# Kernel tuning notes

Hardware: AMD Instinct MI355X
Metric: run time of the kernel (lower is better)

## Reference

```python
import jax, jax.numpy as jnp
import numpy as np

DIM = 96
NUM_HEADS = 3
WIN = 7  # window_size (square)


def _relative_position_index(wh, ww):
    coords = np.stack(np.meshgrid(np.arange(wh), np.arange(ww), indexing='ij'))  # [2, wh, ww]
    flat = coords.reshape(2, -1)  # [2, n]
    rel = flat[:, :, None] - flat[:, None, :]  # [2, n, n]
    rel = rel.transpose(1, 2, 0).astype(np.int64)
    rel[..., 0] += wh - 1
    rel[..., 1] += ww - 1
    rel[..., 0] *= 2 * ww - 1
    return rel.sum(-1)  # [n, n]


def setup_inputs() -> dict:
    key = jax.random.key(0)
    ks = jax.random.split(key, 9)
    b, n, c = 8192, WIN * WIN, DIM
    std = 0.02
    inp = {
        'x': jax.random.normal(ks[0], (b, n, c), jnp.float32),
        'v': jax.random.normal(ks[1], (b, n, c), jnp.float32),
        'w_q': jax.random.normal(ks[2], (c, c), jnp.float32) * std,
        'b_q': jnp.zeros((c,), jnp.float32),
        'w_kv': jax.random.normal(ks[3], (c, 2 * c), jnp.float32) * std,
        'b_kv': jnp.zeros((2 * c,), jnp.float32),
        'w_proj': jax.random.normal(ks[4], (c, c), jnp.float32) * std,
        'b_proj': jnp.zeros((c,), jnp.float32),
        'rpb_table': jax.random.normal(ks[5], ((2 * WIN - 1) * (2 * WIN - 1), NUM_HEADS), jnp.float32) * std,
        'rel_index': jnp.asarray(_relative_position_index(WIN, WIN), jnp.int32),
    }
    return inp


def reference(x, v, w_q, b_q, w_kv, b_kv, w_proj, b_proj, rpb_table, rel_index):
    b, n, c = x.shape
    h = NUM_HEADS
    hd = c // h
    scale = hd ** -0.5
    # q: [b, h, n, hd]
    q = (x @ w_q + b_q).reshape(b, n, h, hd).transpose(0, 2, 1, 3) * scale
    kv = (v @ w_kv + b_kv).reshape(b, n, 2, h, hd)
    k = kv[:, :, 0].transpose(0, 2, 1, 3)  # [b, h, n, hd]
    vv = kv[:, :, 1].transpose(0, 2, 1, 3)
    attn = jnp.einsum('bhqd,bhkd->bhqk', q, k)  # [b, h, n, n]
    bias = rpb_table[rel_index.reshape(-1)].reshape(n, n, h).transpose(2, 0, 1)  # [h, n, n]
    attn = jax.nn.softmax(attn + bias[None], axis=-1)
    out = jnp.einsum('bhqk,bhkd->bhqd', attn, vv).transpose(0, 2, 1, 3).reshape(b, n, c)
    return out @ w_proj + b_proj
```

## Files before the change

### kernel.cpp

```cpp
#include <hip/hip_runtime.h>
#include <hip/hip_bf16.h>

typedef __bf16 bf16x8 __attribute__((ext_vector_type(8)));
typedef float f32x4 __attribute__((ext_vector_type(4)));
typedef short s16x8 __attribute__((ext_vector_type(8)));
typedef short s16x4 __attribute__((ext_vector_type(4)));

#define NTOK 49
#define CDIM 96
#define KS_S 104
#define VT_S 56
#define BN_S 136
#define LOG2E 1.4426950408889634f

#if __has_builtin(__builtin_amdgcn_exp2f)
#define EXP2F(x) __builtin_amdgcn_exp2f(x)
#else
#define EXP2F(x) exp2f(x)
#endif

#define DRAIN() do { asm volatile("s_waitcnt lgkmcnt(0)" ::: "memory"); \
                     __builtin_amdgcn_sched_barrier(0); } while (0)

__device__ __forceinline__ unsigned short f2bf(float f) {
  __hip_bfloat16 h = __float2bfloat16(f);
  return __builtin_bit_cast(unsigned short, h);
}

__device__ __forceinline__ bf16x8 ld_cvt8(const float* p) {
  float4 a = *(const float4*)p;
  float4 b = *(const float4*)(p + 4);
  s16x8 r;
  r[0] = (short)f2bf(a.x); r[1] = (short)f2bf(a.y);
  r[2] = (short)f2bf(a.z); r[3] = (short)f2bf(a.w);
  r[4] = (short)f2bf(b.x); r[5] = (short)f2bf(b.y);
  r[6] = (short)f2bf(b.z); r[7] = (short)f2bf(b.w);
  return __builtin_bit_cast(bf16x8, r);
}

__global__ void prep(const float* __restrict__ wq, const float* __restrict__ wkv,
                     const float* __restrict__ wproj, const float* __restrict__ rpb,
                     const int* __restrict__ relidx, unsigned short* __restrict__ wsT,
                     float* __restrict__ biasf) {
  const int total = 36864 + 3 * 49 * 64;
  for (int i = blockIdx.x * 256 + threadIdx.x; i < total; i += gridDim.x * 256) {
    if (i < 9216) {
      int oc = i / 96, ic = i - oc * 96;
      wsT[i] = f2bf(wq[ic * 96 + oc]);
    } else if (i < 27648) {
      int j = i - 9216; int oc = j / 96, ic = j - oc * 96;
      wsT[i] = f2bf(wkv[ic * 192 + oc]);
    } else if (i < 36864) {
      int j = i - 27648; int oc = j / 96, ic = j - oc * 96;
      wsT[i] = f2bf(wproj[ic * 96 + oc]);
    } else {
      int j = i - 36864; int h = j / 3136; int rc = j - h * 3136;
      int r = rc >> 6, c = rc & 63;
      biasf[j] = (c < 49) ? rpb[relidx[r * 49 + c] * 3 + h] * LOG2E : 0.f;
    }
  }
}

__launch_bounds__(256, 4)
__global__ void attn_fused(const float* __restrict__ xg, const float* __restrict__ vg,
                           const float* __restrict__ bq, const float* __restrict__ bkv,
                           const float* __restrict__ bproj,
                           const unsigned short* __restrict__ wsT,
                           const float* __restrict__ biasf,
                           float* __restrict__ outg) {
  __shared__ __align__(16) unsigned char smem[38352];
  unsigned short* Ks  = (unsigned short*)smem;
  unsigned short* VVT = (unsigned short*)(smem + 10192);

  const int tid = threadIdx.x;
  const int lane = tid & 63;
  const int wv = tid >> 6;
  const int c16 = lane & 15;
  const int g4 = lane >> 4;
  const int win = blockIdx.x;
  const int q0 = (wv == 0) ? 0 : (wv == 1) ? 16 : (wv == 2) ? 32 : 33;
  unsigned short* bnc = (unsigned short*)(smem + 20944) + wv * (16 * BN_S);

  const int mp = wv & 1;
  const bool isK = (wv < 2);
  const int m0 = mp ? 32 : 0;
  const int m1 = mp ? 33 : 16;

  const float* base = xg + (size_t)win * (NTOK * CDIM);
  const float* vbase = vg + (size_t)win * (NTOK * CDIM);
  const float* xrow = base + (q0 + c16) * CDIM;
  const float* vrow0 = vbase + (m0 + c16) * CDIM;
  const float* vrow1 = vbase + (m1 + c16) * CDIM;

  bf16x8 xf[3], vf0[3], vf1[3];
#pragma unroll
  for (int k = 0; k < 3; ++k) {
    xf[k]  = ld_cvt8(xrow  + k * 32 + g4 * 8);
    vf0[k] = ld_cvt8(vrow0 + k * 32 + g4 * 8);
    vf1[k] = ld_cvt8(vrow1 + k * 32 + g4 * 8);
  }

  const float scale = 0.2550348742f;
#pragma unroll
  for (int nt = 0; nt < 6; ++nt) {
    f32x4 acc = {0, 0, 0, 0};
    const int ocl = nt * 16 + c16;
#pragma unroll
    for (int k = 0; k < 3; ++k) {
      bf16x8 b = *(const bf16x8*)(wsT + ocl * 96 + k * 32 + g4 * 8);
      acc = __builtin_amdgcn_mfma_f32_16x16x32_bf16(xf[k], b, acc, 0, 0, 0);
    }
    float bias = bq[ocl];
#pragma unroll
    for (int r = 0; r < 4; ++r)
      bnc[(4 * g4 + r) * BN_S + ocl] = f2bf((acc[r] + bias) * scale);
  }

#pragma unroll
  for (int nt = 0; nt < 6; ++nt) {
    const int ocl = (isK ? 0 : 96) + nt * 16 + c16;
    f32x4 a0 = {0, 0, 0, 0}, a1 = {0, 0, 0, 0};
#pragma unroll
    for (int k = 0; k < 3; ++k) {
      bf16x8 b = *(const bf16x8*)(wsT + 9216 + ocl * 96 + k * 32 + g4 * 8);
      a0 = __builtin_amdgcn_mfma_f32_16x16x32_bf16(vf0[k], b, a0, 0, 0, 0);
      a1 = __builtin_amdgcn_mfma_f32_16x16x32_bf16(vf1[k], b, a1, 0, 0, 0);
    }
    float bias = bkv[ocl];
    if (isK) {
#pragma unroll
      for (int r = 0; r < 4; ++r)
        Ks[(m0 + 4 * g4 + r) * KS_S + ocl] = f2bf(a0[r] + bias);
#pragma unroll
      for (int r = 0; r < 4; ++r)
        Ks[(m1 + 4 * g4 + r) * KS_S + ocl] = f2bf(a1[r] + bias);
    } else {
      int dim = ocl - 96;
      s16x4 p0;
#pragma unroll
      for (int r = 0; r < 4; ++r) p0[r] = (short)f2bf(a0[r] + bias);
      *(s16x4*)(VVT + dim * VT_S + (m0 + 4 * g4)) = p0;
      if (mp == 0) {
        s16x4 p1;
#pragma unroll
        for (int r = 0; r < 4; ++r) p1[r] = (short)f2bf(a1[r] + bias);
        *(s16x4*)(VVT + dim * VT_S + (16 + 4 * g4)) = p1;
      } else {
#pragma unroll
        for (int r = 0; r < 4; ++r)
          VVT[dim * VT_S + 33 + 4 * g4 + r] = f2bf(a1[r] + bias);
      }
    }
  }
  __syncthreads();

  const int q = q0 + c16;

  s16x8 vmask;
#pragma unroll
  for (int j = 0; j < 8; ++j)
    vmask[j] = (short)(((32 + g4 * 8 + j) < 49) ? 0xFFFF : 0x0000);

  f32x4 oacc[6] = {{0,0,0,0},{0,0,0,0},{0,0,0,0},{0,0,0,0},{0,0,0,0},{0,0,0,0}};

  auto softmax_pw = [&](const f32x4* s, const f32x4* bv, int pcol) {
    float vals[16];
#pragma unroll
    for (int kt = 0; kt < 4; ++kt)
#pragma unroll
      for (int r = 0; r < 4; ++r) {
        int key = 16 * kt + 4 * g4 + r;
        vals[kt * 4 + r] = (kt < 3 || key < 49) ? (s[kt][r] + bv[kt][r]) : -1e30f;
      }
    float m8[8];
#pragma unroll
    for (int j = 0; j < 8; ++j) m8[j] = fmaxf(vals[j], vals[j + 8]);
    float ma = fmaxf(m8[0], m8[4]), mb = fmaxf(m8[1], m8[5]);
    float mc = fmaxf(m8[2], m8[6]), md = fmaxf(m8[3], m8[7]);
    float mx = fmaxf(fmaxf(ma, mb), fmaxf(mc, md));
    mx = fmaxf(mx, __shfl_xor(mx, 16, 64));
    mx = fmaxf(mx, __shfl_xor(mx, 32, 64));
    float e[16];
#pragma unroll
    for (int j = 0; j < 16; ++j) e[j] = EXP2F(vals[j] - mx);
    float s8[8];
#pragma unroll
    for (int j = 0; j < 8; ++j) s8[j] = e[j] + e[j + 8];
    float sa = s8[0] + s8[4], sb = s8[1] + s8[5], sc = s8[2] + s8[6], sd = s8[3] + s8[7];
    float sum = (sa + sb) + (sc + sd);
    sum += __shfl_xor(sum, 16, 64);
    sum += __shfl_xor(sum, 32, 64);
    float rinv = 1.0f / sum;
#pragma unroll
    for (int kt = 0; kt < 4; ++kt) {
      s16x4 p;
#pragma unroll
      for (int r = 0; r < 4; ++r) p[r] = (short)f2bf(e[kt * 4 + r] * rinv);
      *(s16x4*)(bnc + c16 * BN_S + pcol + 16 * kt + 4 * g4) = p;
    }
  };

  auto pv_out = [&](int h, int pcol, int ocol) {
    bf16x8 ap0 = *(const bf16x8*)(bnc + c16 * BN_S + pcol + g4 * 8);
    bf16x8 ap1 = *(const bf16x8*)(bnc + c16 * BN_S + pcol + 32 + g4 * 8);
#pragma unroll
    for (int dt = 0; dt < 2; ++dt) {
      int dim = h * 32 + dt * 16 + c16;
      bf16x8 bv0 = *(const bf16x8*)(VVT + dim * VT_S + g4 * 8);
      s16x8 b1 = *(const s16x8*)(VVT + dim * VT_S + 32 + g4 * 8);
      b1 &= vmask;
      f32x4 o = __builtin_amdgcn_mfma_f32_16x16x32_bf16(ap0, bv0, (f32x4){0,0,0,0}, 0, 0, 0);
      o = __builtin_amdgcn_mfma_f32_16x16x32_bf16(ap1, __builtin_bit_cast(bf16x8, b1), o, 0, 0, 0);
#pragma unroll
      for (int r = 0; r < 4; ++r)
        bnc[(4 * g4 + r) * BN_S + ocol + dt * 16 + c16] = f2bf(o[r]);
    }
  };

  auto oproj = [&](int h, int ocol) {
    bf16x8 bo = *(const bf16x8*)(bnc + c16 * BN_S + ocol + g4 * 8);
#pragma unroll
    for (int mt = 0; mt < 6; ++mt) {
      bf16x8 a = *(const bf16x8*)(wsT + 27648 + (mt * 16 + c16) * 96 + h * 32 + g4 * 8);
      oacc[mt] = __builtin_amdgcn_mfma_f32_16x16x32_bf16(a, bo, oacc[mt], 0, 0, 0);
    }
  };

  f32x4 b0v[4], b1v[4];
  {
    const float* br0 = biasf + q * 64 + 4 * g4;
    const float* br1 = biasf + (49 + q) * 64 + 4 * g4;
#pragma unroll
    for (int kt = 0; kt < 4; ++kt) {
      b0v[kt] = *(const f32x4*)(br0 + 16 * kt);
      b1v[kt] = *(const f32x4*)(br1 + 16 * kt);
    }
  }
  bf16x8 qf0 = *(const bf16x8*)(bnc + c16 * BN_S + g4 * 8);
  bf16x8 qf1 = *(const bf16x8*)(bnc + c16 * BN_S + 32 + g4 * 8);
  bf16x8 qf2 = *(const bf16x8*)(bnc + c16 * BN_S + 64 + g4 * 8);

  f32x4 s0[4], s1[4];
#pragma unroll
  for (int kt = 0; kt < 4; ++kt) {
    bf16x8 ak = *(const bf16x8*)(Ks + (16 * kt + c16) * KS_S + g4 * 8);
    s0[kt] = __builtin_amdgcn_mfma_f32_16x16x32_bf16(ak, qf0, (f32x4){0,0,0,0}, 0, 0, 0);
  }
#pragma unroll
  for (int kt = 0; kt < 4; ++kt) {
    bf16x8 ak = *(const bf16x8*)(Ks + (16 * kt + c16) * KS_S + 32 + g4 * 8);
    s1[kt] = __builtin_amdgcn_mfma_f32_16x16x32_bf16(ak, qf1, (f32x4){0,0,0,0}, 0, 0, 0);
  }
  softmax_pw(s0, b0v, 0);
  softmax_pw(s1, b1v, 64);

  f32x4 b2v[4];
  {
    const float* br2 = biasf + (98 + q) * 64 + 4 * g4;
#pragma unroll
    for (int kt = 0; kt < 4; ++kt) b2v[kt] = *(const f32x4*)(br2 + 16 * kt);
  }
  f32x4 s2[4];
#pragma unroll
  for (int kt = 0; kt < 4; ++kt) {
    bf16x8 ak = *(const bf16x8*)(Ks + (16 * kt + c16) * KS_S + 64 + g4 * 8);
    s2[kt] = __builtin_amdgcn_mfma_f32_16x16x32_bf16(ak, qf2, (f32x4){0,0,0,0}, 0, 0, 0);
  }

  DRAIN();
  pv_out(0, 0, 0);
  pv_out(1, 64, 32);
  softmax_pw(s2, b2v, 64);

  DRAIN();
  oproj(0, 0);
  oproj(1, 32);
  pv_out(2, 64, 96);

  DRAIN();
  oproj(2, 96);

  {
    const bool store_ok = (wv < 3) || (c16 == 15);
    float* orow = outg + (size_t)win * (NTOK * CDIM) + q * 96;
#pragma unroll
    for (int mt = 0; mt < 6; ++mt) {
      int oc0 = mt * 16 + g4 * 4;
      if (store_ok) {
        float4 bb = *(const float4*)(bproj + oc0);
        float4 o4;
        o4.x = oacc[mt][0] + bb.x; o4.y = oacc[mt][1] + bb.y;
        o4.z = oacc[mt][2] + bb.z; o4.w = oacc[mt][3] + bb.w;
        *(float4*)(orow + oc0) = o4;
      }
    }
  }
}

extern "C" void kernel_launch(void* const* d_in, const int* in_sizes, int n_in,
                              void* d_out, int out_size, void* d_ws, size_t ws_size,
                              hipStream_t stream) {
  const float* x     = (const float*)d_in[0];
  const float* v     = (const float*)d_in[1];
  const float* wq    = (const float*)d_in[2];
  const float* bq    = (const float*)d_in[3];
  const float* wkv   = (const float*)d_in[4];
  const float* bkv   = (const float*)d_in[5];
  const float* wproj = (const float*)d_in[6];
  const float* bproj = (const float*)d_in[7];
  const float* rpb   = (const float*)d_in[8];
  const int*   relidx= (const int*)d_in[9];
  float* out = (float*)d_out;
  unsigned short* wsT = (unsigned short*)d_ws;
  float* biasf = (float*)((char*)d_ws + 73728);
  int nwin = in_sizes[0] / (NTOK * CDIM);

  hipLaunchKernelGGL(prep, dim3(181), dim3(256), 0, stream,
                     wq, wkv, wproj, rpb, relidx, wsT, biasf);
  hipLaunchKernelGGL(attn_fused, dim3(nwin), dim3(256), 0, stream,
                     x, v, bq, bkv, bproj, wsT, biasf, out);
}
```

Measured before the change: 251.0 us.

## Fuse Q/KV projection loops with weight prefetch, packed bf16 converts, and setprio

```diff
diff --git a/kernel.cpp b/kernel.cpp
--- a/kernel.cpp
+++ b/kernel.cpp
@@ -27,15 +27,27 @@
   return __builtin_bit_cast(unsigned short, h);
 }
 
+__device__ __forceinline__ unsigned int cvtpk(float lo, float hi) {
+  unsigned int r;
+  asm("v_cvt_pk_bf16_f32 %0, %1, %2" : "=v"(r) : "v"(lo), "v"(hi));
+  return r;
+}
+__device__ __forceinline__ unsigned short f2bf_f(float f) {
+  return (unsigned short)cvtpk(f, f);
+}
+__device__ __forceinline__ s16x4 pack4(float a, float b, float c, float d) {
+  union { unsigned int u[2]; s16x4 v; } r;
+  r.u[0] = cvtpk(a, b); r.u[1] = cvtpk(c, d);
+  return r.v;
+}
+
 __device__ __forceinline__ bf16x8 ld_cvt8(const float* p) {
   float4 a = *(const float4*)p;
   float4 b = *(const float4*)(p + 4);
-  s16x8 r;
-  r[0] = (short)f2bf(a.x); r[1] = (short)f2bf(a.y);
-  r[2] = (short)f2bf(a.z); r[3] = (short)f2bf(a.w);
-  r[4] = (short)f2bf(b.x); r[5] = (short)f2bf(b.y);
-  r[6] = (short)f2bf(b.z); r[7] = (short)f2bf(b.w);
-  return __builtin_bit_cast(bf16x8, r);
+  union { unsigned int u[4]; bf16x8 v; } r;
+  r.u[0] = cvtpk(a.x, a.y); r.u[1] = cvtpk(a.z, a.w);
+  r.u[2] = cvtpk(b.x, b.y); r.u[3] = cvtpk(b.z, b.w);
+  return r.v;
 }
 
 __global__ void prep(const float* __restrict__ wq, const float* __restrict__ wkv,
@@ -61,7 +73,7 @@
   }
 }
 
-__launch_bounds__(256, 4)
+__launch_bounds__(256, 3)
 __global__ void attn_fused(const float* __restrict__ xg, const float* __restrict__ vg,
                            const float* __restrict__ bq, const float* __restrict__ bkv,
                            const float* __restrict__ bproj,
@@ -72,11 +84,8 @@
   unsigned short* Ks  = (unsigned short*)smem;
   unsigned short* VVT = (unsigned short*)(smem + 10192);
 
-  const int tid = threadIdx.x;
-  const int lane = tid & 63;
-  const int wv = tid >> 6;
-  const int c16 = lane & 15;
-  const int g4 = lane >> 4;
+  const int tid = threadIdx.x, lane = tid & 63, wv = tid >> 6;
+  const int c16 = lane & 15, g4 = lane >> 4;
   const int win = blockIdx.x;
   const int q0 = (wv == 0) ? 0 : (wv == 1) ? 16 : (wv == 2) ? 32 : 33;
   unsigned short* bnc = (unsigned short*)(smem + 20944) + wv * (16 * BN_S);
@@ -100,62 +109,78 @@
     vf1[k] = ld_cvt8(vrow1 + k * 32 + g4 * 8);
   }
 
+  float bqv[6], bkvv[6];
+#pragma unroll
+  for (int nt = 0; nt < 6; ++nt) {
+    bqv[nt]  = bq[nt * 16 + c16];
+    bkvv[nt] = bkv[(isK ? 0 : 96) + nt * 16 + c16];
+  }
+
   const float scale = 0.2550348742f;
-#pragma unroll
-  for (int nt = 0; nt < 6; ++nt) {
-    f32x4 acc = {0, 0, 0, 0};
-    const int ocl = nt * 16 + c16;
+  const unsigned short* wkvBase = wsT + 9216 + (isK ? 0 : 9216);
+
+  {
+    bf16x8 wqf[2][3], wkf[2][3];
 #pragma unroll
     for (int k = 0; k < 3; ++k) {
-      bf16x8 b = *(const bf16x8*)(wsT + ocl * 96 + k * 32 + g4 * 8);
-      acc = __builtin_amdgcn_mfma_f32_16x16x32_bf16(xf[k], b, acc, 0, 0, 0);
-    }
-    float bias = bq[ocl];
-#pragma unroll
-    for (int r = 0; r < 4; ++r)
-      bnc[(4 * g4 + r) * BN_S + ocl] = f2bf((acc[r] + bias) * scale);
-  }
-
-#pragma unroll
-  for (int nt = 0; nt < 6; ++nt) {
-    const int ocl = (isK ? 0 : 96) + nt * 16 + c16;
-    f32x4 a0 = {0, 0, 0, 0}, a1 = {0, 0, 0, 0};
-#pragma unroll
-    for (int k = 0; k < 3; ++k) {
-      bf16x8 b = *(const bf16x8*)(wsT + 9216 + ocl * 96 + k * 32 + g4 * 8);
-      a0 = __builtin_amdgcn_mfma_f32_16x16x32_bf16(vf0[k], b, a0, 0, 0, 0);
-      a1 = __builtin_amdgcn_mfma_f32_16x16x32_bf16(vf1[k], b, a1, 0, 0, 0);
-    }
-    float bias = bkv[ocl];
-    if (isK) {
-#pragma unroll
-      for (int r = 0; r < 4; ++r)
-        Ks[(m0 + 4 * g4 + r) * KS_S + ocl] = f2bf(a0[r] + bias);
-#pragma unroll
-      for (int r = 0; r < 4; ++r)
-        Ks[(m1 + 4 * g4 + r) * KS_S + ocl] = f2bf(a1[r] + bias);
-    } else {
-      int dim = ocl - 96;
-      s16x4 p0;
-#pragma unroll
-      for (int r = 0; r < 4; ++r) p0[r] = (short)f2bf(a0[r] + bias);
-      *(s16x4*)(VVT + dim * VT_S + (m0 + 4 * g4)) = p0;
-      if (mp == 0) {
-        s16x4 p1;
-#pragma unroll
-        for (int r = 0; r < 4; ++r) p1[r] = (short)f2bf(a1[r] + bias);
-        *(s16x4*)(VVT + dim * VT_S + (16 + 4 * g4)) = p1;
-      } else {
+      wqf[0][k] = *(const bf16x8*)(wsT     + c16 * 96 + k * 32 + g4 * 8);
+      wkf[0][k] = *(const bf16x8*)(wkvBase + c16 * 96 + k * 32 + g4 * 8);
+    }
+#pragma unroll
+    for (int nt = 0; nt < 6; ++nt) {
+      const int cur = nt & 1, nxt = cur ^ 1;
+      if (nt < 5) {
+#pragma unroll
+        for (int k = 0; k < 3; ++k) {
+          wqf[nxt][k] = *(const bf16x8*)(wsT     + ((nt + 1) * 16 + c16) * 96 + k * 32 + g4 * 8);
+          wkf[nxt][k] = *(const bf16x8*)(wkvBase + ((nt + 1) * 16 + c16) * 96 + k * 32 + g4 * 8);
+        }
+      }
+      f32x4 aq = {0,0,0,0}, a0 = {0,0,0,0}, a1 = {0,0,0,0};
+      __builtin_amdgcn_s_setprio(1);
+#pragma unroll
+      for (int k = 0; k < 3; ++k) {
+        aq = __builtin_amdgcn_mfma_f32_16x16x32_bf16(xf[k],  wqf[cur][k], aq, 0, 0, 0);
+        a0 = __builtin_amdgcn_mfma_f32_16x16x32_bf16(vf0[k], wkf[cur][k], a0, 0, 0, 0);
+        a1 = __builtin_amdgcn_mfma_f32_16x16x32_bf16(vf1[k], wkf[cur][k], a1, 0, 0, 0);
+      }
+      __builtin_amdgcn_s_setprio(0);
+      {
+        const int ocl = nt * 16 + c16;
+        float bias = bqv[nt];
 #pragma unroll
         for (int r = 0; r < 4; ++r)
-          VVT[dim * VT_S + 33 + 4 * g4 + r] = f2bf(a1[r] + bias);
+          bnc[(4 * g4 + r) * BN_S + ocl] = f2bf_f((aq[r] + bias) * scale);
+      }
+      {
+        float bias = bkvv[nt];
+        if (isK) {
+          const int ocl = nt * 16 + c16;
+#pragma unroll
+          for (int r = 0; r < 4; ++r)
+            Ks[(m0 + 4 * g4 + r) * KS_S + ocl] = f2bf_f(a0[r] + bias);
+#pragma unroll
+          for (int r = 0; r < 4; ++r)
+            Ks[(m1 + 4 * g4 + r) * KS_S + ocl] = f2bf_f(a1[r] + bias);
+        } else {
+          const int dim = nt * 16 + c16;
+          *(s16x4*)(VVT + dim * VT_S + (m0 + 4 * g4)) =
+              pack4(a0[0] + bias, a0[1] + bias, a0[2] + bias, a0[3] + bias);
+          if (mp == 0) {
+            *(s16x4*)(VVT + dim * VT_S + (16 + 4 * g4)) =
+                pack4(a1[0] + bias, a1[1] + bias, a1[2] + bias, a1[3] + bias);
+          } else {
+#pragma unroll
+            for (int r = 0; r < 4; ++r)
+              VVT[dim * VT_S + 33 + 4 * g4 + r] = f2bf_f(a1[r] + bias);
+          }
+        }
       }
     }
   }
   __syncthreads();
 
   const int q = q0 + c16;
-
   s16x8 vmask;
 #pragma unroll
   for (int j = 0; j < 8; ++j)
@@ -192,38 +217,48 @@
     sum += __shfl_xor(sum, 32, 64);
     float rinv = 1.0f / sum;
 #pragma unroll
-    for (int kt = 0; kt < 4; ++kt) {
-      s16x4 p;
-#pragma unroll
-      for (int r = 0; r < 4; ++r) p[r] = (short)f2bf(e[kt * 4 + r] * rinv);
-      *(s16x4*)(bnc + c16 * BN_S + pcol + 16 * kt + 4 * g4) = p;
-    }
+    for (int kt = 0; kt < 4; ++kt)
+      *(s16x4*)(bnc + c16 * BN_S + pcol + 16 * kt + 4 * g4) =
+          pack4(e[kt*4] * rinv, e[kt*4+1] * rinv, e[kt*4+2] * rinv, e[kt*4+3] * rinv);
   };
 
   auto pv_out = [&](int h, int pcol, int ocol) {
     bf16x8 ap0 = *(const bf16x8*)(bnc + c16 * BN_S + pcol + g4 * 8);
     bf16x8 ap1 = *(const bf16x8*)(bnc + c16 * BN_S + pcol + 32 + g4 * 8);
+    bf16x8 bva[2]; s16x8 bvb[2];
 #pragma unroll
     for (int dt = 0; dt < 2; ++dt) {
       int dim = h * 32 + dt * 16 + c16;
-      bf16x8 bv0 = *(const bf16x8*)(VVT + dim * VT_S + g4 * 8);
-      s16x8 b1 = *(const s16x8*)(VVT + dim * VT_S + 32 + g4 * 8);
-      b1 &= vmask;
-      f32x4 o = __builtin_amdgcn_mfma_f32_16x16x32_bf16(ap0, bv0, (f32x4){0,0,0,0}, 0, 0, 0);
-      o = __builtin_amdgcn_mfma_f32_16x16x32_bf16(ap1, __builtin_bit_cast(bf16x8, b1), o, 0, 0, 0);
+      bva[dt] = *(const bf16x8*)(VVT + dim * VT_S + g4 * 8);
+      s16x8 t = *(const s16x8*)(VVT + dim * VT_S + 32 + g4 * 8);
+      bvb[dt] = t & vmask;
+    }
+    f32x4 o[2];
+    __builtin_amdgcn_s_setprio(1);
+#pragma unroll
+    for (int dt = 0; dt < 2; ++dt) {
+      o[dt] = __builtin_amdgcn_mfma_f32_16x16x32_bf16(ap0, bva[dt], (f32x4){0,0,0,0}, 0, 0, 0);
+      o[dt] = __builtin_amdgcn_mfma_f32_16x16x32_bf16(ap1, __builtin_bit_cast(bf16x8, bvb[dt]), o[dt], 0, 0, 0);
+    }
+    __builtin_amdgcn_s_setprio(0);
+#pragma unroll
+    for (int dt = 0; dt < 2; ++dt)
 #pragma unroll
       for (int r = 0; r < 4; ++r)
-        bnc[(4 * g4 + r) * BN_S + ocol + dt * 16 + c16] = f2bf(o[r]);
-    }
+        bnc[(4 * g4 + r) * BN_S + ocol + dt * 16 + c16] = f2bf_f(o[dt][r]);
   };
 
   auto oproj = [&](int h, int ocol) {
     bf16x8 bo = *(const bf16x8*)(bnc + c16 * BN_S + ocol + g4 * 8);
-#pragma unroll
-    for (int mt = 0; mt < 6; ++mt) {
-      bf16x8 a = *(const bf16x8*)(wsT + 27648 + (mt * 16 + c16) * 96 + h * 32 + g4 * 8);
-      oacc[mt] = __builtin_amdgcn_mfma_f32_16x16x32_bf16(a, bo, oacc[mt], 0, 0, 0);
-    }
+    bf16x8 wa[6];
+#pragma unroll
+    for (int mt = 0; mt < 6; ++mt)
+      wa[mt] = *(const bf16x8*)(wsT + 27648 + (mt * 16 + c16) * 96 + h * 32 + g4 * 8);
+    __builtin_amdgcn_s_setprio(1);
+#pragma unroll
+    for (int mt = 0; mt < 6; ++mt)
+      oacc[mt] = __builtin_amdgcn_mfma_f32_16x16x32_bf16(wa[mt], bo, oacc[mt], 0, 0, 0);
+    __builtin_amdgcn_s_setprio(0);
   };
 
   f32x4 b0v[4], b1v[4];
@@ -241,15 +276,21 @@
   bf16x8 qf2 = *(const bf16x8*)(bnc + c16 * BN_S + 64 + g4 * 8);
 
   f32x4 s0[4], s1[4];
-#pragma unroll
-  for (int kt = 0; kt < 4; ++kt) {
-    bf16x8 ak = *(const bf16x8*)(Ks + (16 * kt + c16) * KS_S + g4 * 8);
-    s0[kt] = __builtin_amdgcn_mfma_f32_16x16x32_bf16(ak, qf0, (f32x4){0,0,0,0}, 0, 0, 0);
-  }
-#pragma unroll
-  for (int kt = 0; kt < 4; ++kt) {
-    bf16x8 ak = *(const bf16x8*)(Ks + (16 * kt + c16) * KS_S + 32 + g4 * 8);
-    s1[kt] = __builtin_amdgcn_mfma_f32_16x16x32_bf16(ak, qf1, (f32x4){0,0,0,0}, 0, 0, 0);
+  {
+    bf16x8 ak0[4], ak1[4];
+#pragma unroll
+    for (int kt = 0; kt < 4; ++kt) {
+      ak0[kt] = *(const bf16x8*)(Ks + (16 * kt + c16) * KS_S + g4 * 8);
+      ak1[kt] = *(const bf16x8*)(Ks + (16 * kt + c16) * KS_S + 32 + g4 * 8);
+    }
+    __builtin_amdgcn_s_setprio(1);
+#pragma unroll
+    for (int kt = 0; kt < 4; ++kt)
+      s0[kt] = __builtin_amdgcn_mfma_f32_16x16x32_bf16(ak0[kt], qf0, (f32x4){0,0,0,0}, 0, 0, 0);
+#pragma unroll
+    for (int kt = 0; kt < 4; ++kt)
+      s1[kt] = __builtin_amdgcn_mfma_f32_16x16x32_bf16(ak1[kt], qf1, (f32x4){0,0,0,0}, 0, 0, 0);
+    __builtin_amdgcn_s_setprio(0);
   }
   softmax_pw(s0, b0v, 0);
   softmax_pw(s1, b1v, 64);
@@ -261,10 +302,16 @@
     for (int kt = 0; kt < 4; ++kt) b2v[kt] = *(const f32x4*)(br2 + 16 * kt);
   }
   f32x4 s2[4];
-#pragma unroll
-  for (int kt = 0; kt < 4; ++kt) {
-    bf16x8 ak = *(const bf16x8*)(Ks + (16 * kt + c16) * KS_S + 64 + g4 * 8);
-    s2[kt] = __builtin_amdgcn_mfma_f32_16x16x32_bf16(ak, qf2, (f32x4){0,0,0,0}, 0, 0, 0);
+  {
+    bf16x8 ak2[4];
+#pragma unroll
+    for (int kt = 0; kt < 4; ++kt)
+      ak2[kt] = *(const bf16x8*)(Ks + (16 * kt + c16) * KS_S + 64 + g4 * 8);
+    __builtin_amdgcn_s_setprio(1);
+#pragma unroll
+    for (int kt = 0; kt < 4; ++kt)
+      s2[kt] = __builtin_amdgcn_mfma_f32_16x16x32_bf16(ak2[kt], qf2, (f32x4){0,0,0,0}, 0, 0, 0);
+    __builtin_amdgcn_s_setprio(0);
   }
 
   DRAIN();
```

Result: no change. 253.9 us (+1.1%).
